# Performance work log

Measured on AMD Instinct MI355X. Metric: run time of the kernel, lower is better.

The kernel has to match this reference:

```python
import jax, jax.numpy as jnp
import numpy as np

# Config matching init_kwargs
PCR = np.array([0.0, -40.0, -3.0], np.float32)          # point_cloud_range min
VSZ = np.array([0.32, 0.32, 4.0], np.float32)            # voxel_size
GRID = np.array([220, 250, 1], np.int32)                 # grid_size
SXYZ, SYZ, SZ = 220 * 250 * 1, 250 * 1, 1                # merge-coord scales
PXY, PY = 220 * 250, 250                                  # pillar scales
X_OFF, Y_OFF, Z_OFF = 0.32 / 2 + 0.0, 0.32 / 2 - 40.0, 4.0 / 2 - 3.0


def _bn(x, g, b, eps=1e-3):
    # BatchNorm1d in training mode: biased batch statistics
    mu = x.mean(0)
    var = x.var(0)
    return (x - mu) / jnp.sqrt(var + eps) * g + b


def setup_inputs() -> dict:
    key = jax.random.key(0)
    N, B = 1_000_000, 4
    ks = jax.random.split(key, 7)
    b = jax.random.randint(ks[0], (N,), 0, B).astype(jnp.float32)
    x = jax.random.uniform(ks[1], (N,), minval=0.0, maxval=70.3)
    y = jax.random.uniform(ks[2], (N,), minval=-40.0, maxval=39.9)
    z = jax.random.uniform(ks[3], (N,), minval=-3.0, maxval=0.9)
    inten = jax.random.uniform(ks[4], (N,))
    points = jnp.stack([b, x, y, z, inten], axis=1)  # [N,5]
    # PFN layer 0: Linear(10->32, no bias) + BN(32); layer 1: Linear(64->128) + BN(128)
    w0 = jax.random.normal(ks[5], (10, 32), jnp.float32) * 0.1
    g0, b0 = jnp.ones((32,), jnp.float32), jnp.zeros((32,), jnp.float32)
    w1 = jax.random.normal(ks[6], (64, 128), jnp.float32) * 0.1
    g1, b1 = jnp.ones((128,), jnp.float32), jnp.zeros((128,), jnp.float32)
    return {"points": points, "w0": w0, "g0": g0, "b0": b0, "w1": w1, "g1": g1, "b1": b1}


def reference(points, w0, g0, b0, w1, g1, b1):
    pcr = jnp.asarray(PCR)
    vsz = jnp.asarray(VSZ)
    grid = jnp.asarray(GRID)
    coords = jnp.floor((points[:, 1:4] - pcr) / vsz).astype(jnp.int32)
    mask = jnp.all((coords >= 0) & (coords < grid), axis=1)
    points = points[mask]
    coords = coords[mask]
    xyz = points[:, 1:4]
    merge = (points[:, 0].astype(jnp.int32) * SXYZ
             + coords[:, 0] * SYZ + coords[:, 1] * SZ + coords[:, 2])
    unq, inv = jnp.unique(merge, return_inverse=True)
    V = int(unq.shape[0])

    cnt = jax.ops.segment_sum(jnp.ones(merge.shape[0], jnp.float32), inv, V)
    mean = jax.ops.segment_sum(xyz, inv, V) / cnt[:, None]  # scatter_mean
    f_cluster = xyz - mean[inv]
    cf = coords.astype(xyz.dtype)
    f_center = jnp.stack([
        xyz[:, 0] - (cf[:, 0] * 0.32 + X_OFF),
        xyz[:, 1] - (cf[:, 1] * 0.32 + Y_OFF),
        xyz[:, 2] - Z_OFF,
    ], axis=1)
    feats = jnp.concatenate([points[:, 1:], f_cluster, f_center], axis=1)  # [N,10]

    # PFN layer 0 (not last): linear -> BN -> relu -> scatter_max -> concat
    x = jax.nn.relu(_bn(feats @ w0, g0, b0))          # [N,32]
    xmax = jax.ops.segment_max(x, inv, V)             # [V,32]
    x = jnp.concatenate([x, xmax[inv]], axis=1)       # [N,64]
    # PFN layer 1 (last): linear -> BN -> relu -> scatter_max
    x = jax.nn.relu(_bn(x @ w1, g1, b1))              # [N,128]
    pillar_feat = jax.ops.segment_max(x, inv, V)      # [V,128]

    u = unq.astype(jnp.int32)
    zeros = jnp.zeros_like(u)
    # stack([b, x, y, 0]) then permute [:, [0,3,2,1]] -> [b, 0, y, x]
    pillar_coords = jnp.stack([u // PXY, zeros, u % PY, (u % PXY) // PY], axis=1)
    return pillar_feat, pillar_coords
```

## Files before the change

kernel.cpp:

```cpp
#include <hip/hip_runtime.h>
#include <cstdint>
#include <cstddef>


constexpr int M_IDS  = 220000;
constexpr int CH     = 256;
constexpr int NCHUNK = (M_IDS + CH - 1) / CH;
constexpr int NB1    = 1024;
constexpr int ELS    = 132;

typedef __attribute__((ext_vector_type(8))) __bf16          bf16x8;
typedef __attribute__((ext_vector_type(8))) unsigned short  u16x8;
typedef __attribute__((ext_vector_type(4))) float           f32x4;

union U8 { u16x8 u; bf16x8 b; };

__device__ __forceinline__ uint16_t f2b(float f) {
    uint32_t u = __float_as_uint(f);
    u += 0x7fffu + ((u >> 16) & 1u);
    return (uint16_t)(u >> 16);
}
__device__ __forceinline__ float b2f(uint16_t h) {
    return __uint_as_float(((uint32_t)h) << 16);
}

__device__ __forceinline__ f32x4 mfma16(bf16x8 a, bf16x8 b, f32x4 c) {
    return __builtin_amdgcn_mfma_f32_16x16x32_bf16(a, b, c, 0, 0, 0);
}

__global__ void k1_count(const float* __restrict__ pts, int* __restrict__ inv,
                         int* __restrict__ cnt, int N)
{
    int i = blockIdx.x * blockDim.x + threadIdx.x;
    if (i >= N) return;
    const float* p = pts + (size_t)i * 5;
    float b = p[0], x = p[1], y = p[2], z = p[3];
    float fx = floorf((x - 0.0f) / 0.32f);
    float fy = floorf((y + 40.0f) / 0.32f);
    float fz = floorf((z + 3.0f) / 4.0f);
    bool ok = (fx >= 0.0f) && (fx < 220.0f) && (fy >= 0.0f) && (fy < 250.0f) &&
              (fz >= 0.0f) && (fz < 1.0f);
    if (!ok) { inv[i] = -1; return; }
    int m = (int)b * 55000 + (int)fx * 250 + (int)fy + (int)fz;
    inv[i] = m;
    atomicAdd(&cnt[m], 1);
}

__global__ void k2a_tot(const int* __restrict__ cnt, int* __restrict__ totO,
                        int* __restrict__ totC, int* __restrict__ np)
{
    __shared__ int so[CH], sc[CH];
    int t = threadIdx.x;
    int id = blockIdx.x * CH + t;
    int c = (id < M_IDS) ? cnt[id] : 0;
    so[t] = (c > 0) ? 1 : 0;
    sc[t] = c;
    __syncthreads();
    for (int s = CH / 2; s > 0; s >>= 1) {
        if (t < s) { so[t] += so[t + s]; sc[t] += sc[t + s]; }
        __syncthreads();
    }
    if (t == 0) { totO[blockIdx.x] = so[0]; totC[blockIdx.x] = sc[0]; atomicAdd(np, sc[0]); }
}

__global__ void k2b_scan(const int* __restrict__ totO, const int* __restrict__ totC,
                         int* __restrict__ baseO, int* __restrict__ baseC)
{
    __shared__ int a[1024], bb[1024];
    int t = threadIdx.x;
    int vo = (t < NCHUNK) ? totO[t] : 0;
    int vc = (t < NCHUNK) ? totC[t] : 0;
    a[t] = vo; bb[t] = vc;
    __syncthreads();
    for (int off = 1; off < 1024; off <<= 1) {
        int xa = (t >= off) ? a[t - off] : 0;
        int xb = (t >= off) ? bb[t - off] : 0;
        __syncthreads();
        a[t] += xa; bb[t] += xb;
        __syncthreads();
    }
    baseO[t] = a[t] - vo;
    baseC[t] = bb[t] - vc;
}

__global__ void k2c_index(const int* __restrict__ cnt, const int* __restrict__ baseO,
                          const int* __restrict__ baseC, int* __restrict__ idxArr,
                          int* __restrict__ bOff, int* __restrict__ vOff,
                          int* __restrict__ vCnt, float* __restrict__ outCoords)
{
    __shared__ int a[CH], bb[CH];
    int t = threadIdx.x;
    int id = blockIdx.x * CH + t;
    int c = (id < M_IDS) ? cnt[id] : 0;
    int occ = (c > 0) ? 1 : 0;
    a[t] = occ; bb[t] = c;
    __syncthreads();
    for (int off = 1; off < CH; off <<= 1) {
        int xa = (t >= off) ? a[t - off] : 0;
        int xb = (t >= off) ? bb[t - off] : 0;
        __syncthreads();
        a[t] += xa; bb[t] += xb;
        __syncthreads();
    }
    if (id >= M_IDS) return;
    int g  = baseO[blockIdx.x] + a[t] - occ;
    int bo = baseC[blockIdx.x] + bb[t] - c;
    idxArr[id] = g;
    bOff[id]   = bo;
    if (occ) {
        vOff[g] = bo;
        vCnt[g] = c;
        int b2 = id / 55000;
        int rm = id % 55000;
        int cx = rm / 250;
        int cy = rm % 250;
        outCoords[(size_t)g * 4 + 0] = (float)b2;
        outCoords[(size_t)g * 4 + 1] = 0.0f;
        outCoords[(size_t)g * 4 + 2] = (float)cy;
        outCoords[(size_t)g * 4 + 3] = (float)cx;
    }
}

__global__ void k3_order(const float* __restrict__ pts, const int* __restrict__ inv,
                         const int* __restrict__ bOff, const int* __restrict__ idxArr,
                         int* __restrict__ cursor, float4* __restrict__ pts4,
                         int* __restrict__ vS, int N)
{
    int i = blockIdx.x * blockDim.x + threadIdx.x;
    if (i >= N) return;
    int m = inv[i];
    if (m < 0) return;
    const float* p = pts + (size_t)i * 5;
    float x = p[1], y = p[2], z = p[3], it = p[4];
    int slot = atomicAdd(&cursor[m], 1);
    int j = bOff[m] + slot;
    pts4[j] = make_float4(x, y, z, it);
    vS[j]   = idxArr[m];
}

__global__ void k4_mean(const float4* __restrict__ pts4, const int* __restrict__ vOff,
                        const int* __restrict__ vCnt, float* __restrict__ meanArr, int V)
{
    int g = blockIdx.x * blockDim.x + threadIdx.x;
    if (g >= V) return;
    int off = vOff[g], c = vCnt[g];
    float sx = 0.0f, sy = 0.0f, sz = 0.0f;
    for (int p = 0; p < c; p++) {
        float4 q = pts4[off + p];
        sx += q.x; sy += q.y; sz += q.z;
    }
    float fc = (float)c;
    meanArr[(size_t)g * 3 + 0] = sx / fc;
    meanArr[(size_t)g * 3 + 1] = sy / fc;
    meanArr[(size_t)g * 3 + 2] = sz / fc;
}

__global__ __launch_bounds__(256)
void k5_y0(const float4* __restrict__ pts4, const float* __restrict__ w0,
           const int* __restrict__ vS, const float* __restrict__ meanArr,
           uint16_t* __restrict__ XpL, float* __restrict__ stats0, int Npad)
{
    __shared__ float sl[64];
    int t = threadIdx.x;
    if (t < 64) sl[t] = 0.0f;
    __syncthreads();
    float s[32], q[32];
#pragma unroll
    for (int c = 0; c < 32; c++) { s[c] = 0.0f; q[c] = 0.0f; }

    for (int j = blockIdx.x * 256 + t; j < Npad; j += gridDim.x * 256) {
        float y0[32];
#pragma unroll
        for (int c = 0; c < 32; c++) y0[c] = 0.0f;
        int v = vS[j];
        if (v >= 0) {
            float4 P = pts4[j];
            float x = P.x, y = P.y, z = P.z, it = P.w;
            float fx = floorf((x - 0.0f) / 0.32f);
            float fy = floorf((y + 40.0f) / 0.32f);
            float f[10];
            f[0] = x; f[1] = y; f[2] = z; f[3] = it;
            f[4] = x - meanArr[(size_t)v * 3 + 0];
            f[5] = y - meanArr[(size_t)v * 3 + 1];
            f[6] = z - meanArr[(size_t)v * 3 + 2];
            f[7] = x - (fx * 0.32f + 0.16f);
            f[8] = y - (fy * 0.32f - 39.84f);
            f[9] = z + 1.0f;
#pragma unroll
            for (int d = 0; d < 10; d++) {
                float fd = f[d];
#pragma unroll
                for (int c = 0; c < 32; c++) y0[c] += fd * w0[d * 32 + c];
            }
        }
        uint32_t pk[16];
#pragma unroll
        for (int k = 0; k < 16; k++)
            pk[k] = (uint32_t)f2b(y0[2 * k]) | ((uint32_t)f2b(y0[2 * k + 1]) << 16);
        uint4* rp = (uint4*)(XpL + (size_t)j * 32);
#pragma unroll
        for (int k = 0; k < 4; k++)
            rp[k] = make_uint4(pk[4 * k], pk[4 * k + 1], pk[4 * k + 2], pk[4 * k + 3]);
#pragma unroll
        for (int c = 0; c < 32; c++) { s[c] += y0[c]; q[c] += y0[c] * y0[c]; }
    }

    int lane = t & 63;
#pragma unroll
    for (int c = 0; c < 32; c++) {
#pragma unroll
        for (int m = 1; m < 64; m <<= 1) {
            s[c] += __shfl_xor(s[c], m);
            q[c] += __shfl_xor(q[c], m);
        }
        if (lane == c) {
            atomicAdd(&sl[c],      s[c]);
            atomicAdd(&sl[32 + c], q[c]);
        }
    }
    __syncthreads();
    if (t < 64) atomicAdd(&stats0[t], sl[t]);
}

__global__ void k_bnfin(const float* __restrict__ stats, const int* __restrict__ np,
                        const float* __restrict__ g, const float* __restrict__ b,
                        float* __restrict__ sb, int C)
{
    int c = blockIdx.x * blockDim.x + threadIdx.x;
    if (c >= C) return;
    float n   = (float)(*np);
    float mu  = stats[c] / n;
    float var = stats[C + c] / n - mu * mu;
    float s   = g[c] / sqrtf(var + 1e-3f);
    sb[c]     = s;
    sb[C + c] = b[c] - mu * s;
}

__global__ __launch_bounds__(256)
void k8_xmax(uint16_t* __restrict__ XpL, uint16_t* __restrict__ XpU,
             const int* __restrict__ vOff, const int* __restrict__ vCnt,
             const float* __restrict__ sb0, int V)
{
    int t = threadIdx.x;
    int g = blockIdx.x * 4 + (t >> 6);
    if (g >= V) return;
    int lane = t & 63;
    int c = lane & 31, h = lane >> 5;
    float sc = sb0[c], bc = sb0[32 + c];
    int off = vOff[g], n = vCnt[g];
    float m = 0.0f;
    for (int i = h; i < n; i += 2) {
        size_t a = (size_t)(off + i) * 32 + c;
        float e = fmaxf(b2f(XpL[a]) * sc + bc, 0.0f);
        XpL[a] = f2b(e);
        m = fmaxf(m, e);
    }
    m = fmaxf(m, __shfl_xor(m, 32));
    uint16_t mb = f2b(m);
    for (int i = h; i < n; i += 2)
        XpU[(size_t)(off + i) * 32 + c] = mb;
}

__device__ __forceinline__ void load_wsplit(const float* __restrict__ w1, int cb,
                                            int l15, int lg, bf16x8* Bhi, bf16x8* Blo)
{
    int col = cb + l15;
    int kr  = lg * 8;
#pragma unroll
    for (int nb = 0; nb < 4; nb++) {
#pragma unroll
        for (int ks = 0; ks < 2; ks++) {
            U8 h, l;
#pragma unroll
            for (int jj = 0; jj < 8; jj++) {
                float w = w1[(ks * 32 + kr + jj) * 128 + col + nb * 16];
                uint16_t hb = f2b(w);
                h.u[jj] = hb;
                l.u[jj] = f2b(w - b2f(hb));
            }
            Bhi[nb * 2 + ks] = h.b;
            Blo[nb * 2 + ks] = l.b;
        }
    }
}

__global__ __launch_bounds__(256)
void kB_mapply(const uint16_t* __restrict__ XpL, const uint16_t* __restrict__ XpU,
               const float* __restrict__ w1, const float* __restrict__ g1,
               const int* __restrict__ vS, const int* __restrict__ vOff,
               const int* __restrict__ vCnt, const int* __restrict__ np,
               unsigned int* __restrict__ out, float* __restrict__ sPart, int ntiles)
{
    __shared__ float els[64 * ELS];
    int t = threadIdx.x;
    int wv = t >> 6, lane = t & 63;
    int l15 = lane & 15, lg = lane >> 4;
    int rowSel = wv & 1;
    int cb     = (wv >> 1) * 64;

    bf16x8 Bhi[8], Blo[8];
    load_wsplit(w1, cb, l15, lg, Bhi, Blo);

    int nv = *np;
    int cg = t & 127;
    int slot = t >> 7;
    uint32_t sgnm = (g1[cg] < 0.0f) ? 0x80000000u : 0u;
    float ssum = 0.0f, qsum = 0.0f;

    for (int tile = blockIdx.x; tile < ntiles; tile += gridDim.x) {
        int tb = tile * 64;
        if (tb >= nv) break;
        int rbase = tb + rowSel * 32;
        f32x4 acc[2][4];
#pragma unroll
        for (int m = 0; m < 2; m++)
#pragma unroll
            for (int nb = 0; nb < 4; nb++)
                acc[m][nb] = (f32x4){0.0f, 0.0f, 0.0f, 0.0f};
#pragma unroll
        for (int m = 0; m < 2; m++) {
            size_t r = (size_t)(rbase + m * 16 + l15);
            U8 tL, tU;
            tL.u = *(const u16x8*)(XpL + r * 32 + lg * 8);
            tU.u = *(const u16x8*)(XpU + r * 32 + lg * 8);
#pragma unroll
            for (int nb = 0; nb < 4; nb++) {
                acc[m][nb] = mfma16(tL.b, Bhi[nb * 2],     acc[m][nb]);
                acc[m][nb] = mfma16(tL.b, Blo[nb * 2],     acc[m][nb]);
                acc[m][nb] = mfma16(tU.b, Bhi[nb * 2 + 1], acc[m][nb]);
                acc[m][nb] = mfma16(tU.b, Blo[nb * 2 + 1], acc[m][nb]);
            }
        }
        __syncthreads();
#pragma unroll
        for (int m = 0; m < 2; m++) {
            int rloc = rowSel * 32 + m * 16 + lg * 4;
#pragma unroll
            for (int nb = 0; nb < 4; nb++) {
                int c = cb + nb * 16 + l15;
#pragma unroll
                for (int r = 0; r < 4; r++)
                    els[(rloc + r) * ELS + c] = acc[m][nb][r];
            }
        }
        __syncthreads();
        int lastRow = nv - 1 - tb; if (lastRow > 63) lastRow = 63;
        int gFirst = vS[tb];
        int gLast  = vS[tb + lastRow];
        for (int g = gFirst + slot; g <= gLast; g += 2) {
            int off = vOff[g], end = off + vCnt[g];
            int a  = off > tb ? off : tb;
            int e2 = end < tb + 64 ? end : tb + 64;
            float mx = __uint_as_float(0xff800000u);
            for (int p2 = a; p2 < e2; p2++) {
                float v = els[(p2 - tb) * ELS + cg];
                ssum += v; qsum += v * v;
                mx = fmaxf(mx, __uint_as_float(__float_as_uint(v) ^ sgnm));
            }
            uint32_t u = __float_as_uint(mx);
            uint32_t enc = (u & 0x80000000u) ? ~u : (u | 0x80000000u);
            size_t oa = (size_t)g * 128 + cg;
            if (off >= tb && end <= tb + 64) out[oa] = enc;
            else atomicMax(&out[oa], enc);
        }
    }
    __syncthreads();
    els[t] = ssum; els[256 + t] = qsum;
    __syncthreads();
    if (t < 128) {
        sPart[(size_t)cg * NB1 + blockIdx.x]         = els[t] + els[t + 128];
        sPart[(size_t)(128 + cg) * NB1 + blockIdx.x] = els[256 + t] + els[256 + t + 128];
    }
}

__global__ void k_red1(const float* __restrict__ part, float* __restrict__ stats1)
{
    __shared__ float red[4];
    int o = blockIdx.x, t = threadIdx.x;
    float s = 0.0f;
    for (int k = t; k < NB1; k += 256) s += part[(size_t)o * NB1 + k];
#pragma unroll
    for (int m = 1; m < 64; m <<= 1) s += __shfl_xor(s, m);
    if ((t & 63) == 0) red[t >> 6] = s;
    __syncthreads();
    if (t == 0) stats1[o] = red[0] + red[1] + red[2] + red[3];
}

__global__ void k_final(unsigned int* __restrict__ out, const float* __restrict__ sb1,
                        const float* __restrict__ g1, int n4)
{
    int i = blockIdx.x * 256 + threadIdx.x;
    if (i >= n4) return;
    uint4 e = ((const uint4*)out)[i];
    int c0 = (i & 31) * 4;
    uint32_t ee[4] = {e.x, e.y, e.z, e.w};
    float r[4];
#pragma unroll
    for (int j = 0; j < 4; j++) {
        int c = c0 + j;
        uint32_t u = (ee[j] & 0x80000000u) ? (ee[j] ^ 0x80000000u) : ~ee[j];
        float f = __uint_as_float(u);
        uint32_t sg = (g1[c] < 0.0f) ? 0x80000000u : 0u;
        f = __uint_as_float(__float_as_uint(f) ^ sg);
        r[j] = fmaxf(f * sb1[c] + sb1[128 + c], 0.0f);
    }
    ((float4*)out)[i] = make_float4(r[0], r[1], r[2], r[3]);
}

extern "C" void kernel_launch(void* const* d_in, const int* in_sizes, int n_in,
                              void* d_out, int out_size, void* d_ws, size_t ws_size,
                              hipStream_t stream)
{
    const float* pts = (const float*)d_in[0];
    const float* w0  = (const float*)d_in[1];
    const float* g0  = (const float*)d_in[2];
    const float* b0  = (const float*)d_in[3];
    const float* w1  = (const float*)d_in[4];
    const float* g1  = (const float*)d_in[5];
    const float* b1  = (const float*)d_in[6];

    int N      = in_sizes[0] / 5;
    int V      = out_size / 132;
    int Npad   = (N + 255) & ~255;
    int ntiles = Npad / 64;

    char* ws = (char*)d_ws;
    size_t off = 0;
    auto alloc = [&](size_t bytes) { size_t r = off; off = (off + bytes + 255) & ~(size_t)255; return r; };

    int*    inv     = (int*)(ws + alloc((size_t)N * 4));
    float4* pts4    = (float4*)(ws + alloc((size_t)Npad * 16));
    int*    vS      = (int*)(ws + alloc((size_t)Npad * 4));
    size_t  zOff    = off;
    int*    cnt     = (int*)(ws + alloc((size_t)M_IDS * 4));
    int*    cursor  = (int*)(ws + alloc((size_t)M_IDS * 4));
    float*  stats   = (float*)(ws + alloc(320 * 4));
    int*    np      = (int*)(ws + alloc(4));
    size_t  zBytes  = off - zOff;
    int*    bOff    = (int*)(ws + alloc((size_t)M_IDS * 4));
    int*    idxArr  = (int*)(ws + alloc((size_t)M_IDS * 4));
    int*    vOff    = (int*)(ws + alloc((size_t)M_IDS * 4));
    int*    vCnt    = (int*)(ws + alloc((size_t)M_IDS * 4));
    int*    totO    = (int*)(ws + alloc(1024 * 4));
    int*    totC    = (int*)(ws + alloc(1024 * 4));
    int*    baseO   = (int*)(ws + alloc(1024 * 4));
    int*    baseC   = (int*)(ws + alloc(1024 * 4));
    float*  sb0     = (float*)(ws + alloc(64 * 4));
    float*  sb1     = (float*)(ws + alloc(256 * 4));
    float*  sPart   = (float*)(ws + alloc((size_t)256 * NB1 * 4));
    float*  meanArr = (float*)(ws + alloc((size_t)V * 12));
    uint16_t* XpL   = (uint16_t*)(ws + alloc((size_t)Npad * 32 * 2));
    uint16_t* XpU   = (uint16_t*)(ws + alloc((size_t)Npad * 32 * 2));
    (void)ws_size;

    hipMemsetAsync(ws + zOff, 0, zBytes, stream);
    hipMemsetAsync(vS, 0xFF, (size_t)Npad * 4, stream);
    hipMemsetAsync(d_out, 0, (size_t)V * 128 * 4, stream);

    int blocksN = (N + 255) / 256;
    float* outF = (float*)d_out;

    k1_count<<<blocksN, 256, 0, stream>>>(pts, inv, cnt, N);
    k2a_tot<<<NCHUNK, CH, 0, stream>>>(cnt, totO, totC, np);
    k2b_scan<<<1, 1024, 0, stream>>>(totO, totC, baseO, baseC);
    k2c_index<<<NCHUNK, CH, 0, stream>>>(cnt, baseO, baseC, idxArr, bOff, vOff, vCnt,
                                         outF + (size_t)V * 128);
    k3_order<<<blocksN, 256, 0, stream>>>(pts, inv, bOff, idxArr, cursor, pts4, vS, N);
    k4_mean<<<(V + 255) / 256, 256, 0, stream>>>(pts4, vOff, vCnt, meanArr, V);
    k5_y0<<<512, 256, 0, stream>>>(pts4, w0, vS, meanArr, XpL, stats, Npad);
    k_bnfin<<<1, 32, 0, stream>>>(stats, np, g0, b0, sb0, 32);
    k8_xmax<<<(V + 3) / 4, 256, 0, stream>>>(XpL, XpU, vOff, vCnt, sb0, V);
    kB_mapply<<<NB1, 256, 0, stream>>>(XpL, XpU, w1, g1, vS, vOff, vCnt, np,
                                       (unsigned int*)d_out, sPart, ntiles);
    k_red1<<<256, 256, 0, stream>>>(sPart, stats + 64);
    k_bnfin<<<1, 128, 0, stream>>>(stats + 64, np, g1, b1, sb1, 128);
    k_final<<<(V * 32 + 255) / 256, 256, 0, stream>>>((unsigned int*)d_out, sb1, g1, V * 32);
}
```

Before: 598.4 us.

## Fuse point ordering with layer-0 features, drop per-point xmax buffer

New measurement: 818.8 us. 1.37x slower.

```diff
diff --git a/kernel.cpp b/kernel.cpp
--- a/kernel.cpp
+++ b/kernel.cpp
@@ -6,8 +6,8 @@
 constexpr int M_IDS  = 220000;
 constexpr int CH     = 256;
 constexpr int NCHUNK = (M_IDS + CH - 1) / CH;
-constexpr int NB1    = 1024;
-constexpr int ELS    = 132;
+constexpr int NB1    = 1536;
+constexpr int ELS2   = 132;
 
 typedef __attribute__((ext_vector_type(8))) __bf16          bf16x8;
 typedef __attribute__((ext_vector_type(8))) unsigned short  u16x8;
@@ -29,7 +29,7 @@
 }
 
 __global__ void k1_count(const float* __restrict__ pts, int* __restrict__ inv,
-                         int* __restrict__ cnt, int N)
+                         int* __restrict__ cnt, float* __restrict__ sums, int N)
 {
     int i = blockIdx.x * blockDim.x + threadIdx.x;
     if (i >= N) return;
@@ -44,6 +44,9 @@
     int m = (int)b * 55000 + (int)fx * 250 + (int)fy + (int)fz;
     inv[i] = m;
     atomicAdd(&cnt[m], 1);
+    atomicAdd(&sums[(size_t)m * 4 + 0], x);
+    atomicAdd(&sums[(size_t)m * 4 + 1], y);
+    atomicAdd(&sums[(size_t)m * 4 + 2], z);
 }
 
 __global__ void k2a_tot(const int* __restrict__ cnt, int* __restrict__ totO,
@@ -84,9 +87,10 @@
 }
 
 __global__ void k2c_index(const int* __restrict__ cnt, const int* __restrict__ baseO,
-                          const int* __restrict__ baseC, int* __restrict__ idxArr,
-                          int* __restrict__ bOff, int* __restrict__ vOff,
-                          int* __restrict__ vCnt, float* __restrict__ outCoords)
+                          const int* __restrict__ baseC, const float* __restrict__ sums,
+                          int* __restrict__ idxArr, int* __restrict__ bOff,
+                          int* __restrict__ vOff, int* __restrict__ vCnt,
+                          float4* __restrict__ meanArr, float* __restrict__ outCoords)
 {
     __shared__ int a[CH], bb[CH];
     int t = threadIdx.x;
@@ -110,6 +114,9 @@
     if (occ) {
         vOff[g] = bo;
         vCnt[g] = c;
+        float ic = 1.0f / (float)c;
+        const float* sm = sums + (size_t)id * 4;
+        meanArr[g] = make_float4(sm[0] * ic, sm[1] * ic, sm[2] * ic, 0.0f);
         int b2 = id / 55000;
         int rm = id % 55000;
         int cx = rm / 250;
@@ -121,44 +128,12 @@
     }
 }
 
-__global__ void k3_order(const float* __restrict__ pts, const int* __restrict__ inv,
-                         const int* __restrict__ bOff, const int* __restrict__ idxArr,
-                         int* __restrict__ cursor, float4* __restrict__ pts4,
-                         int* __restrict__ vS, int N)
-{
-    int i = blockIdx.x * blockDim.x + threadIdx.x;
-    if (i >= N) return;
-    int m = inv[i];
-    if (m < 0) return;
-    const float* p = pts + (size_t)i * 5;
-    float x = p[1], y = p[2], z = p[3], it = p[4];
-    int slot = atomicAdd(&cursor[m], 1);
-    int j = bOff[m] + slot;
-    pts4[j] = make_float4(x, y, z, it);
-    vS[j]   = idxArr[m];
-}
-
-__global__ void k4_mean(const float4* __restrict__ pts4, const int* __restrict__ vOff,
-                        const int* __restrict__ vCnt, float* __restrict__ meanArr, int V)
-{
-    int g = blockIdx.x * blockDim.x + threadIdx.x;
-    if (g >= V) return;
-    int off = vOff[g], c = vCnt[g];
-    float sx = 0.0f, sy = 0.0f, sz = 0.0f;
-    for (int p = 0; p < c; p++) {
-        float4 q = pts4[off + p];
-        sx += q.x; sy += q.y; sz += q.z;
-    }
-    float fc = (float)c;
-    meanArr[(size_t)g * 3 + 0] = sx / fc;
-    meanArr[(size_t)g * 3 + 1] = sy / fc;
-    meanArr[(size_t)g * 3 + 2] = sz / fc;
-}
-
 __global__ __launch_bounds__(256)
-void k5_y0(const float4* __restrict__ pts4, const float* __restrict__ w0,
-           const int* __restrict__ vS, const float* __restrict__ meanArr,
-           uint16_t* __restrict__ XpL, float* __restrict__ stats0, int Npad)
+void k35_feat(const float* __restrict__ pts, const float* __restrict__ w0,
+              const int* __restrict__ inv, const int* __restrict__ bOff,
+              const int* __restrict__ idxArr, const float4* __restrict__ meanArr,
+              int* __restrict__ cursor, uint16_t* __restrict__ XpL,
+              int* __restrict__ vS, float* __restrict__ stats0, int N)
 {
     __shared__ float sl[64];
     int t = threadIdx.x;
@@ -168,39 +143,42 @@
 #pragma unroll
     for (int c = 0; c < 32; c++) { s[c] = 0.0f; q[c] = 0.0f; }
 
-    for (int j = blockIdx.x * 256 + t; j < Npad; j += gridDim.x * 256) {
+    for (int i = blockIdx.x * 256 + t; i < N; i += gridDim.x * 256) {
+        int m = inv[i];
+        if (m < 0) continue;
+        const float* p = pts + (size_t)i * 5;
+        float x = p[1], y = p[2], z = p[3], it = p[4];
+        int slot = atomicAdd(&cursor[m], 1);
+        int j = bOff[m] + slot;
+        int v = idxArr[m];
+        float4 mn = meanArr[v];
+        float fx = floorf(x / 0.32f);
+        float fy = floorf((y + 40.0f) / 0.32f);
+        float f[10];
+        f[0] = x; f[1] = y; f[2] = z; f[3] = it;
+        f[4] = x - mn.x; f[5] = y - mn.y; f[6] = z - mn.z;
+        f[7] = x - (fx * 0.32f + 0.16f);
+        f[8] = y - (fy * 0.32f - 39.84f);
+        f[9] = z + 1.0f;
         float y0[32];
 #pragma unroll
         for (int c = 0; c < 32; c++) y0[c] = 0.0f;
-        int v = vS[j];
-        if (v >= 0) {
-            float4 P = pts4[j];
-            float x = P.x, y = P.y, z = P.z, it = P.w;
-            float fx = floorf((x - 0.0f) / 0.32f);
-            float fy = floorf((y + 40.0f) / 0.32f);
-            float f[10];
-            f[0] = x; f[1] = y; f[2] = z; f[3] = it;
-            f[4] = x - meanArr[(size_t)v * 3 + 0];
-            f[5] = y - meanArr[(size_t)v * 3 + 1];
-            f[6] = z - meanArr[(size_t)v * 3 + 2];
-            f[7] = x - (fx * 0.32f + 0.16f);
-            f[8] = y - (fy * 0.32f - 39.84f);
-            f[9] = z + 1.0f;
-#pragma unroll
-            for (int d = 0; d < 10; d++) {
-                float fd = f[d];
-#pragma unroll
-                for (int c = 0; c < 32; c++) y0[c] += fd * w0[d * 32 + c];
-            }
+#pragma unroll
+        for (int d = 0; d < 10; d++) {
+            float fd = f[d];
+#pragma unroll
+            for (int c = 0; c < 32; c++) y0[c] += fd * w0[d * 32 + c];
         }
         uint32_t pk[16];
 #pragma unroll
         for (int k = 0; k < 16; k++)
             pk[k] = (uint32_t)f2b(y0[2 * k]) | ((uint32_t)f2b(y0[2 * k + 1]) << 16);
         uint4* rp = (uint4*)(XpL + (size_t)j * 32);
-#pragma unroll
-        for (int k = 0; k < 4; k++)
-            rp[k] = make_uint4(pk[4 * k], pk[4 * k + 1], pk[4 * k + 2], pk[4 * k + 3]);
+        rp[0] = make_uint4(pk[0], pk[1], pk[2], pk[3]);
+        rp[1] = make_uint4(pk[4], pk[5], pk[6], pk[7]);
+        rp[2] = make_uint4(pk[8], pk[9], pk[10], pk[11]);
+        rp[3] = make_uint4(pk[12], pk[13], pk[14], pk[15]);
+        vS[j] = v;
 #pragma unroll
         for (int c = 0; c < 32; c++) { s[c] += y0[c]; q[c] += y0[c] * y0[c]; }
     }
@@ -209,14 +187,11 @@
 #pragma unroll
     for (int c = 0; c < 32; c++) {
 #pragma unroll
-        for (int m = 1; m < 64; m <<= 1) {
-            s[c] += __shfl_xor(s[c], m);
-            q[c] += __shfl_xor(q[c], m);
-        }
-        if (lane == c) {
-            atomicAdd(&sl[c],      s[c]);
-            atomicAdd(&sl[32 + c], q[c]);
-        }
+        for (int m2 = 1; m2 < 64; m2 <<= 1) {
+            s[c] += __shfl_xor(s[c], m2);
+            q[c] += __shfl_xor(q[c], m2);
+        }
+        if (lane == c) { atomicAdd(&sl[c], s[c]); atomicAdd(&sl[32 + c], q[c]); }
     }
     __syncthreads();
     if (t < 64) atomicAdd(&stats0[t], sl[t]);
@@ -237,28 +212,31 @@
 }
 
 __global__ __launch_bounds__(256)
-void k8_xmax(uint16_t* __restrict__ XpL, uint16_t* __restrict__ XpU,
-             const int* __restrict__ vOff, const int* __restrict__ vCnt,
-             const float* __restrict__ sb0, int V)
+void k8_xmax(const uint16_t* __restrict__ XpL, const int* __restrict__ vOff,
+             const int* __restrict__ vCnt, const float* __restrict__ sb0,
+             uint32_t* __restrict__ xmaxV, int V)
 {
     int t = threadIdx.x;
     int g = blockIdx.x * 4 + (t >> 6);
     if (g >= V) return;
     int lane = t & 63;
-    int c = lane & 31, h = lane >> 5;
-    float sc = sb0[c], bc = sb0[32 + c];
+    int c2 = lane & 15, h = lane >> 4;
+    int ch0 = c2 * 2;
+    float sA = sb0[ch0],     bA = sb0[32 + ch0];
+    float sB = sb0[ch0 + 1], bB = sb0[33 + ch0];
     int off = vOff[g], n = vCnt[g];
-    float m = 0.0f;
-    for (int i = h; i < n; i += 2) {
-        size_t a = (size_t)(off + i) * 32 + c;
-        float e = fmaxf(b2f(XpL[a]) * sc + bc, 0.0f);
-        XpL[a] = f2b(e);
-        m = fmaxf(m, e);
-    }
-    m = fmaxf(m, __shfl_xor(m, 32));
-    uint16_t mb = f2b(m);
-    for (int i = h; i < n; i += 2)
-        XpU[(size_t)(off + i) * 32 + c] = mb;
+    float m0 = 0.0f, m1 = 0.0f;
+    for (int i = h; i < n; i += 4) {
+        uint32_t u = *(const uint32_t*)(XpL + (size_t)(off + i) * 32 + ch0);
+        float e0 = fmaxf(b2f((uint16_t)u) * sA + bA, 0.0f);
+        float e1 = fmaxf(b2f((uint16_t)(u >> 16)) * sB + bB, 0.0f);
+        m0 = fmaxf(m0, e0);
+        m1 = fmaxf(m1, e1);
+    }
+    m0 = fmaxf(m0, __shfl_xor(m0, 16)); m0 = fmaxf(m0, __shfl_xor(m0, 32));
+    m1 = fmaxf(m1, __shfl_xor(m1, 16)); m1 = fmaxf(m1, __shfl_xor(m1, 32));
+    if (h == 0)
+        xmaxV[(size_t)g * 16 + c2] = (uint32_t)f2b(m0) | ((uint32_t)f2b(m1) << 16);
 }
 
 __device__ __forceinline__ void load_wsplit(const float* __restrict__ w1, int cb,
@@ -285,13 +263,15 @@
 }
 
 __global__ __launch_bounds__(256)
-void kB_mapply(const uint16_t* __restrict__ XpL, const uint16_t* __restrict__ XpU,
+void kB_mapply(const uint16_t* __restrict__ XpL, const uint16_t* __restrict__ xmaxV,
                const float* __restrict__ w1, const float* __restrict__ g1,
                const int* __restrict__ vS, const int* __restrict__ vOff,
                const int* __restrict__ vCnt, const int* __restrict__ np,
-               unsigned int* __restrict__ out, float* __restrict__ sPart, int ntiles)
-{
-    __shared__ float els[64 * ELS];
+               const float* __restrict__ sb0, unsigned int* __restrict__ out,
+               float* __restrict__ sPart, int ntiles)
+{
+    __shared__ uint16_t els[64 * ELS2];
+    __shared__ int sVS[64];
     int t = threadIdx.x;
     int wv = t >> 6, lane = t & 63;
     int l15 = lane & 15, lg = lane >> 4;
@@ -301,37 +281,76 @@
     bf16x8 Bhi[8], Blo[8];
     load_wsplit(w1, cb, l15, lg, Bhi, Blo);
 
+    float sc0[8], bc0[8];
+#pragma unroll
+    for (int j = 0; j < 8; j++) { sc0[j] = sb0[lg * 8 + j]; bc0[j] = sb0[32 + lg * 8 + j]; }
+
     int nv = *np;
     int cg = t & 127;
-    int slot = t >> 7;
+    int half = t >> 7;
+    int r0h = half * 32;
     uint32_t sgnm = (g1[cg] < 0.0f) ? 0x80000000u : 0u;
-    float ssum = 0.0f, qsum = 0.0f;
-
-    for (int tile = blockIdx.x; tile < ntiles; tile += gridDim.x) {
+    float s[4] = {0.f, 0.f, 0.f, 0.f}, q[4] = {0.f, 0.f, 0.f, 0.f};
+
+    U8 pL[2], pU[2];
+    int pvs = 0;
+    int tile = blockIdx.x;
+    if (tile < ntiles && tile * 64 < nv) {
+        int tb2 = tile * 64;
+        int r0 = tb2 + rowSel * 32 + l15;
+        int v0 = vS[r0];
+        int v1 = vS[r0 + 16];
+        pL[0].u = *(const u16x8*)(XpL + (size_t)r0 * 32 + lg * 8);
+        pL[1].u = *(const u16x8*)(XpL + (size_t)(r0 + 16) * 32 + lg * 8);
+        if (t < 64) pvs = vS[tb2 + t];
+        v0 = (r0 < nv) ? v0 : 0;
+        v1 = (r0 + 16 < nv) ? v1 : 0;
+        pU[0].u = *(const u16x8*)(xmaxV + (size_t)v0 * 32 + lg * 8);
+        pU[1].u = *(const u16x8*)(xmaxV + (size_t)v1 * 32 + lg * 8);
+    }
+
+    for (; tile < ntiles; tile += gridDim.x) {
         int tb = tile * 64;
         if (tb >= nv) break;
-        int rbase = tb + rowSel * 32;
+        U8 aL[2], aU[2];
+#pragma unroll
+        for (int m = 0; m < 2; m++) {
+            int r = tb + rowSel * 32 + m * 16 + l15;
+            bool live = (r < nv);
+#pragma unroll
+            for (int j = 0; j < 8; j++) {
+                float e = fmaxf(b2f(pL[m].u[j]) * sc0[j] + bc0[j], 0.0f);
+                aL[m].u[j] = live ? f2b(e) : (uint16_t)0;
+                aU[m].u[j] = live ? pU[m].u[j] : (uint16_t)0;
+            }
+        }
         f32x4 acc[2][4];
 #pragma unroll
         for (int m = 0; m < 2; m++)
 #pragma unroll
             for (int nb = 0; nb < 4; nb++)
-                acc[m][nb] = (f32x4){0.0f, 0.0f, 0.0f, 0.0f};
+                acc[m][nb] = (f32x4){0.f, 0.f, 0.f, 0.f};
 #pragma unroll
         for (int m = 0; m < 2; m++) {
-            size_t r = (size_t)(rbase + m * 16 + l15);
-            U8 tL, tU;
-            tL.u = *(const u16x8*)(XpL + r * 32 + lg * 8);
-            tU.u = *(const u16x8*)(XpU + r * 32 + lg * 8);
 #pragma unroll
             for (int nb = 0; nb < 4; nb++) {
-                acc[m][nb] = mfma16(tL.b, Bhi[nb * 2],     acc[m][nb]);
-                acc[m][nb] = mfma16(tL.b, Blo[nb * 2],     acc[m][nb]);
-                acc[m][nb] = mfma16(tU.b, Bhi[nb * 2 + 1], acc[m][nb]);
-                acc[m][nb] = mfma16(tU.b, Blo[nb * 2 + 1], acc[m][nb]);
+                acc[m][nb] = mfma16(aL[m].b, Bhi[nb * 2],     acc[m][nb]);
+                acc[m][nb] = mfma16(aL[m].b, Blo[nb * 2],     acc[m][nb]);
+                acc[m][nb] = mfma16(aU[m].b, Bhi[nb * 2 + 1], acc[m][nb]);
+                acc[m][nb] = mfma16(aU[m].b, Blo[nb * 2 + 1], acc[m][nb]);
             }
         }
-        __syncthreads();
+#pragma unroll
+        for (int m = 0; m < 2; m++)
+#pragma unroll
+            for (int nb = 0; nb < 4; nb++)
+#pragma unroll
+                for (int r = 0; r < 4; r++) {
+                    float y = acc[m][nb][r];
+                    s[nb] += y; q[nb] += y * y;
+                }
+        __syncthreads();
+        if (t < 64) sVS[t] = pvs;
 #pragma unroll
         for (int m = 0; m < 2; m++) {
             int rloc = rowSel * 32 + m * 16 + lg * 4;
@@ -340,36 +359,71 @@
                 int c = cb + nb * 16 + l15;
 #pragma unroll
                 for (int r = 0; r < 4; r++)
-                    els[(rloc + r) * ELS + c] = acc[m][nb][r];
+                    els[(rloc + r) * ELS2 + c] = f2b(acc[m][nb][r]);
             }
         }
         __syncthreads();
+        int tp = tile + gridDim.x;
+        if (tp < ntiles && tp * 64 < nv) {
+            int tb2 = tp * 64;
+            int r0 = tb2 + rowSel * 32 + l15;
+            int v0 = vS[r0];
+            int v1 = vS[r0 + 16];
+            pL[0].u = *(const u16x8*)(XpL + (size_t)r0 * 32 + lg * 8);
+            pL[1].u = *(const u16x8*)(XpL + (size_t)(r0 + 16) * 32 + lg * 8);
+            if (t < 64) pvs = vS[tb2 + t];
+            v0 = (r0 < nv) ? v0 : 0;
+            v1 = (r0 + 16 < nv) ? v1 : 0;
+            pU[0].u = *(const u16x8*)(xmaxV + (size_t)v0 * 32 + lg * 8);
+            pU[1].u = *(const u16x8*)(xmaxV + (size_t)v1 * 32 + lg * 8);
+        }
         int lastRow = nv - 1 - tb; if (lastRow > 63) lastRow = 63;
-        int gFirst = vS[tb];
-        int gLast  = vS[tb + lastRow];
-        for (int g = gFirst + slot; g <= gLast; g += 2) {
-            int off = vOff[g], end = off + vCnt[g];
-            int a  = off > tb ? off : tb;
-            int e2 = end < tb + 64 ? end : tb + 64;
+        int r1h = (r0h + 32 <= lastRow + 1) ? (r0h + 32) : (lastRow + 1);
+        if (r0h < r1h) {
+            int curg = sVS[r0h];
             float mx = __uint_as_float(0xff800000u);
-            for (int p2 = a; p2 < e2; p2++) {
-                float v = els[(p2 - tb) * ELS + cg];
-                ssum += v; qsum += v * v;
-                mx = fmaxf(mx, __uint_as_float(__float_as_uint(v) ^ sgnm));
+            for (int p2 = r0h; p2 < r1h; p2++) {
+                int vg = sVS[p2];
+                if (vg != curg) {
+                    int offv = vOff[curg], endv = offv + vCnt[curg];
+                    uint32_t u = __float_as_uint(mx);
+                    uint32_t enc = (u & 0x80000000u) ? ~u : (u | 0x80000000u);
+                    size_t oa = (size_t)curg * 128 + cg;
+                    if (offv >= tb + r0h && endv <= tb + r1h) out[oa] = enc;
+                    else atomicMax(&out[oa], enc);
+                    curg = vg;
+                    mx = __uint_as_float(0xff800000u);
+                }
+                uint32_t raw = ((uint32_t)els[p2 * ELS2 + cg]) << 16;
+                mx = fmaxf(mx, __uint_as_float(raw ^ sgnm));
             }
+            int offv = vOff[curg], endv = offv + vCnt[curg];
             uint32_t u = __float_as_uint(mx);
             uint32_t enc = (u & 0x80000000u) ? ~u : (u | 0x80000000u);
-            size_t oa = (size_t)g * 128 + cg;
-            if (off >= tb && end <= tb + 64) out[oa] = enc;
+            size_t oa = (size_t)curg * 128 + cg;
+            if (offv >= tb + r0h && endv <= tb + r1h) out[oa] = enc;
             else atomicMax(&out[oa], enc);
         }
     }
     __syncthreads();
-    els[t] = ssum; els[256 + t] = qsum;
+    float* fl = (float*)els;
+#pragma unroll
+    for (int nb = 0; nb < 4; nb++) {
+        s[nb] += __shfl_xor(s[nb], 16); s[nb] += __shfl_xor(s[nb], 32);
+        q[nb] += __shfl_xor(q[nb], 16); q[nb] += __shfl_xor(q[nb], 32);
+    }
+    if (lane < 16) {
+#pragma unroll
+        for (int nb = 0; nb < 4; nb++) {
+            int ch = cb + nb * 16 + lane;
+            fl[rowSel * 128 + ch]       = s[nb];
+            fl[256 + rowSel * 128 + ch] = q[nb];
+        }
+    }
     __syncthreads();
     if (t < 128) {
-        sPart[(size_t)cg * NB1 + blockIdx.x]         = els[t] + els[t + 128];
-        sPart[(size_t)(128 + cg) * NB1 + blockIdx.x] = els[256 + t] + els[256 + t + 128];
+        sPart[(size_t)t * NB1 + blockIdx.x]         = fl[t] + fl[128 + t];
+        sPart[(size_t)(128 + t) * NB1 + blockIdx.x] = fl[256 + t] + fl[384 + t];
     }
 }
 
@@ -429,13 +483,13 @@
     auto alloc = [&](size_t bytes) { size_t r = off; off = (off + bytes + 255) & ~(size_t)255; return r; };
 
     int*    inv     = (int*)(ws + alloc((size_t)N * 4));
-    float4* pts4    = (float4*)(ws + alloc((size_t)Npad * 16));
     int*    vS      = (int*)(ws + alloc((size_t)Npad * 4));
     size_t  zOff    = off;
     int*    cnt     = (int*)(ws + alloc((size_t)M_IDS * 4));
     int*    cursor  = (int*)(ws + alloc((size_t)M_IDS * 4));
     float*  stats   = (float*)(ws + alloc(320 * 4));
     int*    np      = (int*)(ws + alloc(4));
+    float*  sums    = (float*)(ws + alloc((size_t)M_IDS * 16));
     size_t  zBytes  = off - zOff;
     int*    bOff    = (int*)(ws + alloc((size_t)M_IDS * 4));
     int*    idxArr  = (int*)(ws + alloc((size_t)M_IDS * 4));
@@ -448,30 +502,30 @@
     float*  sb0     = (float*)(ws + alloc(64 * 4));
     float*  sb1     = (float*)(ws + alloc(256 * 4));
     float*  sPart   = (float*)(ws + alloc((size_t)256 * NB1 * 4));
-    float*  meanArr = (float*)(ws + alloc((size_t)V * 12));
+    float4* meanArr = (float4*)(ws + alloc((size_t)V * 16));
     uint16_t* XpL   = (uint16_t*)(ws + alloc((size_t)Npad * 32 * 2));
-    uint16_t* XpU   = (uint16_t*)(ws + alloc((size_t)Npad * 32 * 2));
+    uint16_t* xmaxV = (uint16_t*)(ws + alloc((size_t)V * 32 * 2));
     (void)ws_size;
 
     hipMemsetAsync(ws + zOff, 0, zBytes, stream);
-    hipMemsetAsync(vS, 0xFF, (size_t)Npad * 4, stream);
     hipMemsetAsync(d_out, 0, (size_t)V * 128 * 4, stream);
 
     int blocksN = (N + 255) / 256;
     float* outF = (float*)d_out;
 
-    k1_count<<<blocksN, 256, 0, stream>>>(pts, inv, cnt, N);
+    k1_count<<<blocksN, 256, 0, stream>>>(pts, inv, cnt, sums, N);
     k2a_tot<<<NCHUNK, CH, 0, stream>>>(cnt, totO, totC, np);
     k2b_scan<<<1, 1024, 0, stream>>>(totO, totC, baseO, baseC);
-    k2c_index<<<NCHUNK, CH, 0, stream>>>(cnt, baseO, baseC, idxArr, bOff, vOff, vCnt,
+    k2c_index<<<NCHUNK, CH, 0, stream>>>(cnt, baseO, baseC, sums, idxArr, bOff,
+                                         vOff, vCnt, meanArr,
                                          outF + (size_t)V * 128);
-    k3_order<<<blocksN, 256, 0, stream>>>(pts, inv, bOff, idxArr, cursor, pts4, vS, N);
-    k4_mean<<<(V + 255) / 256, 256, 0, stream>>>(pts4, vOff, vCnt, meanArr, V);
-    k5_y0<<<512, 256, 0, stream>>>(pts4, w0, vS, meanArr, XpL, stats, Npad);
+    k35_feat<<<1024, 256, 0, stream>>>(pts, w0, inv, bOff, idxArr, meanArr,
+                                       cursor, XpL, vS, stats, N);
     k_bnfin<<<1, 32, 0, stream>>>(stats, np, g0, b0, sb0, 32);
-    k8_xmax<<<(V + 3) / 4, 256, 0, stream>>>(XpL, XpU, vOff, vCnt, sb0, V);
-    kB_mapply<<<NB1, 256, 0, stream>>>(XpL, XpU, w1, g1, vS, vOff, vCnt, np,
-                                       (unsigned int*)d_out, sPart, ntiles);
+    k8_xmax<<<(V + 3) / 4, 256, 0, stream>>>(XpL, vOff, vCnt, sb0,
+                                             (uint32_t*)xmaxV, V);
+    kB_mapply<<<NB1, 256, 0, stream>>>(XpL, xmaxV, w1, g1, vS, vOff, vCnt, np,
+                                       sb0, (unsigned int*)d_out, sPart, ntiles);
     k_red1<<<256, 256, 0, stream>>>(sPart, stats + 64);
     k_bnfin<<<1, 128, 0, stream>>>(stats + 64, np, g1, b1, sb1, 128);
     k_final<<<(V * 32 + 255) / 256, 256, 0, stream>>>((unsigned int*)d_out, sb1, g1, V * 32);
```
